# Performance work log

Measured on AMD Instinct MI355X. Metric: run time of the kernel, lower is better.

The kernel has to match this reference:

```python
import jax, jax.numpy as jnp
import numpy as np

N_TOKEN = 256
C_PAIR = 128
C = 32
N_HEADS = 4
LN_EPS = 1e-5


def setup_inputs() -> dict:
    key = jax.random.key(0)
    ks = jax.random.split(key, 8)
    w = lambda k, shape: jax.random.normal(k, shape, dtype=jnp.float32) * 0.02
    return {
        "pair": jax.random.normal(ks[0], (N_TOKEN, N_TOKEN, C_PAIR), dtype=jnp.float32),
        "gamma": jnp.ones((C_PAIR,), dtype=jnp.float32),
        "beta": jnp.zeros((C_PAIR,), dtype=jnp.float32),
        "Wq": w(ks[1], (C_PAIR, C * N_HEADS)),
        "Wk": w(ks[2], (C_PAIR, C * N_HEADS)),
        "Wv": w(ks[3], (C_PAIR, C * N_HEADS)),
        "Wb": w(ks[4], (C_PAIR, N_HEADS)),
        "Wg": w(ks[5], (C_PAIR, C * N_HEADS)),
        "Wout": w(ks[6], (C * N_HEADS, C_PAIR)),
    }


def _layernorm(x, gamma, beta):
    mu = jnp.mean(x, axis=-1, keepdims=True)
    var = jnp.mean(jnp.square(x - mu), axis=-1, keepdims=True)
    return (x - mu) * jax.lax.rsqrt(var + LN_EPS) * gamma + beta


def reference(pair, gamma, beta, Wq, Wk, Wv, Wb, Wg, Wout):
    n = pair.shape[0]
    pn = _layernorm(pair, gamma, beta)  # [N, N, c_pair]
    q = (pn @ Wq).reshape(n, n, N_HEADS, C)  # [i, j, h, c]
    k = (pn @ Wk).reshape(n, n, N_HEADS, C)  # [i, k, h, c]
    v = (pn @ Wv).reshape(n, n, N_HEADS, C)
    b = pn @ Wb                               # [j, k, h] pairwise bias
    g = jax.nn.sigmoid(pn @ Wg).reshape(n, n, N_HEADS, C)
    # a^h_ijk = softmax_k( q_ij . k_ik / sqrt(c) + b_jk )
    logits = jnp.einsum("ijhc,ikhc->ijkh", q, k) / np.float32(np.sqrt(C))
    logits = logits + b[None, :, :, :]        # broadcast over i: bias indexed by (j, k)
    attn = jax.nn.softmax(logits, axis=2)     # softmax over k axis
    o = jnp.einsum("ijkh,ikhc->ijhc", attn, v) * g
    return o.reshape(n, n, N_HEADS * C) @ Wout  # [N, N, c_pair]
```

## Files before the change

### kernel.cpp

```cpp
#include <hip/hip_runtime.h>

#define N_TOK 256
#define CP    128
#define CHD   32
#define NH    4
#define NT    65536
#define NCOL  528

typedef short short8 __attribute__((ext_vector_type(8)));
typedef float f32x4  __attribute__((ext_vector_type(4)));
typedef float f32x2  __attribute__((ext_vector_type(2)));

__device__ __forceinline__ short f2bf(float f) {
    unsigned u = __builtin_bit_cast(unsigned, f);
    u += 0x7fffu + ((u >> 16) & 1u);
    return (short)(u >> 16);
}
__device__ __forceinline__ float bf2f(short s) {
    unsigned u = ((unsigned)(unsigned short)s) << 16;
    return __builtin_bit_cast(float, u);
}

__global__ void pack_weights(const float* __restrict__ Wq, const float* __restrict__ Wk,
                             const float* __restrict__ Wv, const float* __restrict__ Wb,
                             const float* __restrict__ Wg, const float* __restrict__ Wout,
                             short* __restrict__ wcat, short* __restrict__ woutT) {
    int idx = blockIdx.x * 256 + threadIdx.x;
    if (idx < NCOL * CP) {
        int n = idx >> 7, k = idx & 127;
        float v = 0.f;
        if (n < 512) {
            const float* W = (n < 128) ? Wq : (n < 256) ? Wk : (n < 384) ? Wv : Wg;
            int col = (n & 96) + 2 * (n & 15) + ((n >> 4) & 1);
            v = W[k * 128 + col];
            if (n < 128) v *= 0.17677669529663687f;
        } else if (n < 516) {
            v = Wb[k * 4 + (n - 512)];
        }
        wcat[n * CP + k] = f2bf(v);
    } else {
        int j = idx - NCOL * CP;
        if (j < 128 * 128) {
            int n = j >> 7, k = j & 127;
            int col = (n & 96) + 2 * (n & 15) + ((n >> 4) & 1);
            woutT[n * 128 + k] = f2bf(Wout[k * 128 + col]);
        }
    }
}

__global__ __launch_bounds__(256, 4)
void ln_proj(const float* __restrict__ pair, const float* __restrict__ gamma,
             const float* __restrict__ beta, const short* __restrict__ wcat,
             short* __restrict__ qt, short* __restrict__ kt,
             short* __restrict__ vt, short* __restrict__ gt,
             float* __restrict__ bt) {
    __shared__ short pn[10240];
    const int tid = threadIdx.x;
    const int wv = tid >> 6, lane = tid & 63;
    const int quad = lane >> 4, l15 = lane & 15;
    const int r0 = blockIdx.x * 64;
    short* const ST = &pn[wv * 2560];

    float ga0 = gamma[2 * lane], ga1 = gamma[2 * lane + 1];
    float be0 = beta[2 * lane],  be1 = beta[2 * lane + 1];

    #pragma unroll 4
    for (int rr = 0; rr < 16; ++rr) {
        int row = wv * 16 + rr;
        const float* src = pair + (size_t)(r0 + row) * CP + 2 * lane;
        float x0 = src[0], x1 = src[1];
        float s = x0 + x1;
        #pragma unroll
        for (int m = 32; m; m >>= 1) s += __shfl_xor(s, m);
        float mu = s * (1.f / 128.f);
        float d0 = x0 - mu, d1 = x1 - mu;
        float vs = d0 * d0 + d1 * d1;
        #pragma unroll
        for (int m = 32; m; m >>= 1) vs += __shfl_xor(vs, m);
        float rs = rsqrtf(vs * (1.f / 128.f) + 1e-5f);
        short y0 = f2bf(d0 * rs * ga0 + be0);
        short y1 = f2bf(d1 * rs * ga1 + be1);
        unsigned pk = ((unsigned)(unsigned short)y0) | (((unsigned)(unsigned short)y1) << 16);
        *(unsigned*)&pn[row * 136 + 2 * lane] = pk;
    }
    __syncthreads();

    short8 af[4][4];
    #pragma unroll
    for (int rt = 0; rt < 4; ++rt)
        #pragma unroll
        for (int s = 0; s < 4; ++s)
            af[rt][s] = *(const short8*)&pn[(rt * 16 + l15) * 136 + s * 32 + quad * 8];
    __syncthreads();

    short* const dst = (wv == 0) ? qt : (wv == 1) ? kt : (wv == 2) ? vt : gt;

#define LOADB(BUF, CHN) {                                                          \
        int n_ = (CHN) * 16 + l15;                                                 \
        _Pragma("unroll")                                                          \
        for (int s = 0; s < 4; ++s)                                                \
            BUF[s] = *(const short8*)&wcat[(size_t)n_ * CP + s * 32 + quad * 8];   \
    }

#define EVEN(BUF) {                                                                \
        _Pragma("unroll")                                                          \
        for (int rt = 0; rt < 4; ++rt) {                                           \
            f32x4 a = {0.f, 0.f, 0.f, 0.f};                                        \
            _Pragma("unroll")                                                      \
            for (int s = 0; s < 4; ++s)                                            \
                a = __builtin_amdgcn_mfma_f32_16x16x32_bf16(af[rt][s], BUF[s], a, 0, 0, 0); \
            accE[rt] = a;                                                          \
        }                                                                          \
    }

#define ODD(CC, BUF) {                                                             \
        const int chn = wv * 8 + (CC);                                             \
        const int h_ = (chn >> 1) & 3;                                             \
        _Pragma("unroll")                                                          \
        for (int rt = 0; rt < 4; ++rt) {                                           \
            f32x4 a = {0.f, 0.f, 0.f, 0.f};                                        \
            _Pragma("unroll")                                                      \
            for (int s = 0; s < 4; ++s)                                            \
                a = __builtin_amdgcn_mfma_f32_16x16x32_bf16(af[rt][s], BUF[s], a, 0, 0, 0); \
            _Pragma("unroll")                                                      \
            for (int r = 0; r < 4; ++r) {                                          \
                int rowl = rt * 16 + quad * 4 + r;                                 \
                float ve = accE[rt][r], vo = a[r];                                 \
                if (wv == 3) {                                                     \
                    ve = 1.f / (1.f + __expf(-ve));                                \
                    vo = 1.f / (1.f + __expf(-vo));                                \
                }                                                                  \
                unsigned pk = ((unsigned)(unsigned short)f2bf(ve))                 \
                            | (((unsigned)(unsigned short)f2bf(vo)) << 16);        \
                *(unsigned*)&ST[rowl * 40 + 2 * l15] = pk;                         \
            }                                                                      \
        }                                                                          \
        const size_t hb2 = (size_t)h_ * NT * CHD + (size_t)r0 * CHD;               \
        _Pragma("unroll")                                                          \
        for (int s = 0; s < 4; ++s) {                                              \
            int f = s * 64 + lane;                                                 \
            int row = f >> 2, cs = (f & 3) * 8;                                    \
            short8 v = *(const short8*)&ST[row * 40 + cs];                         \
            *(short8*)(dst + hb2 + (size_t)row * CHD + cs) = v;                    \
        }                                                                          \
    }

    short8 bA[4], bB[4];
    f32x4 accE[4];
    LOADB(bA, wv * 8 + 0)
    LOADB(bB, wv * 8 + 1)
    EVEN(bA) LOADB(bA, wv * 8 + 2)
    ODD(1, bB) LOADB(bB, wv * 8 + 3)
    EVEN(bA) LOADB(bA, wv * 8 + 4)
    ODD(3, bB) LOADB(bB, wv * 8 + 5)
    EVEN(bA) LOADB(bA, wv * 8 + 6)
    ODD(5, bB) LOADB(bB, wv * 8 + 7)
    EVEN(bA) LOADB(bA, wv * 8 + 8)
    ODD(7, bB)

    if (wv == 3) {
        #pragma unroll
        for (int rt = 0; rt < 4; ++rt) {
            f32x4 acc = {0.f, 0.f, 0.f, 0.f};
            #pragma unroll
            for (int s = 0; s < 4; ++s)
                acc = __builtin_amdgcn_mfma_f32_16x16x32_bf16(af[rt][s], bA[s], acc, 0, 0, 0);
            if (l15 < 4) {
                #pragma unroll
                for (int r = 0; r < 4; ++r) {
                    int gr = r0 + rt * 16 + quad * 4 + r;
                    bt[l15 * NT + gr] = acc[r];
                }
            }
        }
    }
#undef LOADB
#undef EVEN
#undef ODD
}

__global__ __launch_bounds__(256)
void bias_T(const float* __restrict__ bt, float* __restrict__ btT) {
    __shared__ float t[64][65];
    int bid = blockIdx.x;
    int h = bid >> 4, tj = (bid >> 2) & 3, tk = bid & 3;
    const float* src = bt + (size_t)h * NT;
    float* dstp = btT + (size_t)h * NT;
    int c = threadIdx.x & 63, r4 = threadIdx.x >> 6;
    #pragma unroll
    for (int rr = 0; rr < 16; ++rr) {
        int r = rr * 4 + r4;
        t[r][c] = src[(size_t)(tj * 64 + r) * 256 + tk * 64 + c];
    }
    __syncthreads();
    #pragma unroll
    for (int rr = 0; rr < 16; ++rr) {
        int k = rr * 4 + r4;
        dstp[(size_t)(tk * 64 + k) * 256 + tj * 64 + c] = t[c][k];
    }
}

__global__ __launch_bounds__(256)
void attn(const short* __restrict__ qt, const short* __restrict__ kt,
          const short* __restrict__ vt, const short* __restrict__ gt,
          const float* __restrict__ btT, short* __restrict__ og) {
    __shared__ short vT[32 * 264];
    __shared__ short pl[64 * 264];
    const int tid = threadIdx.x;
    const int h = blockIdx.x >> 8, i = blockIdx.x & 255;
    const int wv = tid >> 6, lane = tid & 63;
    const int quad = lane >> 4, l15 = lane & 15;

    const short* kbase = kt + ((size_t)h * NT + (size_t)i * 256) * CHD;
    const short* vbase = vt + ((size_t)h * NT + (size_t)i * 256) * CHD;
    const short* qbase = qt + ((size_t)h * NT + (size_t)i * 256) * CHD;
    const short* gbase = gt + ((size_t)h * NT + (size_t)i * 256) * CHD;
    const float* btTb = btT + (size_t)h * NT;

    for (int g = tid; g < 1024; g += 256) {
        int key = g >> 2, p = g & 3;
        short8 s = *(const short8*)(vbase + key * CHD + p * 8);
        #pragma unroll
        for (int cc = 0; cc < 8; ++cc) {
            int c = p * 8 + cc;
            int row = (c & 1) ? 16 + (c >> 1) : (c >> 1);
            vT[row * 264 + key] = s[cc];
        }
    }
    __syncthreads();

    for (int jt = 0; jt < 4; ++jt) {
        int jbase = jt * 64 + wv * 16;
        short8 aq = *(const short8*)(qbase + (jbase + l15) * CHD + quad * 8);

        f32x4 sacc[16];
        __builtin_amdgcn_s_setprio(1);
        #pragma unroll
        for (int t = 0; t < 16; ++t) {
            f32x4 c = *(const f32x4*)(btTb + (size_t)(t * 16 + l15) * 256 + jbase + quad * 4);
            short8 bk = *(const short8*)(kbase + (t * 16 + l15) * CHD + quad * 8);
            sacc[t] = __builtin_amdgcn_mfma_f32_16x16x32_bf16(aq, bk, c, 0, 0, 0);
        }
        __builtin_amdgcn_s_setprio(0);
        float mx[4] = {-1e30f, -1e30f, -1e30f, -1e30f}, sm[4] = {0.f, 0.f, 0.f, 0.f};
        #pragma unroll
        for (int t = 0; t < 16; ++t)
            #pragma unroll
            for (int r = 0; r < 4; ++r) mx[r] = fmaxf(mx[r], sacc[t][r]);
        #pragma unroll
        for (int m = 1; m < 16; m <<= 1)
            #pragma unroll
            for (int r = 0; r < 4; ++r) mx[r] = fmaxf(mx[r], __shfl_xor(mx[r], m, 16));
        #pragma unroll
        for (int t = 0; t < 16; ++t)
            #pragma unroll
            for (int r = 0; r < 4; ++r) {
                float e = __expf(sacc[t][r] - mx[r]);
                sacc[t][r] = e;
                sm[r] += e;
            }
        #pragma unroll
        for (int m = 1; m < 16; m <<= 1)
            #pragma unroll
            for (int r = 0; r < 4; ++r) sm[r] += __shfl_xor(sm[r], m, 16);
        float inv[4];
        #pragma unroll
        for (int r = 0; r < 4; ++r) inv[r] = 1.f / sm[r];
        #pragma unroll
        for (int t = 0; t < 16; ++t)
            #pragma unroll
            for (int r = 0; r < 4; ++r)
                pl[(wv * 16 + quad * 4 + r) * 264 + t * 16 + l15] = f2bf(sacc[t][r] * inv[r]);
        f32x4 oacc[2];
        oacc[0] = f32x4{0.f, 0.f, 0.f, 0.f};
        oacc[1] = f32x4{0.f, 0.f, 0.f, 0.f};
        __builtin_amdgcn_s_setprio(1);
        #pragma unroll
        for (int ks = 0; ks < 8; ++ks) {
            short8 ap = *(const short8*)&pl[(wv * 16 + l15) * 264 + ks * 32 + quad * 8];
            #pragma unroll
            for (int nt = 0; nt < 2; ++nt) {
                short8 bv = *(const short8*)&vT[(nt * 16 + l15) * 264 + ks * 32 + quad * 8];
                oacc[nt] = __builtin_amdgcn_mfma_f32_16x16x32_bf16(ap, bv, oacc[nt], 0, 0, 0);
            }
        }
        __builtin_amdgcn_s_setprio(0);
        #pragma unroll
        for (int r = 0; r < 4; ++r) {
            int j = jbase + quad * 4 + r;
            unsigned gw = *(const unsigned*)(gbase + (size_t)j * CHD + 2 * l15);
            float g0 = bf2f((short)(gw & 0xffff));
            float g1 = bf2f((short)(gw >> 16));
            unsigned pk = ((unsigned)(unsigned short)f2bf(oacc[0][r] * g0))
                        | (((unsigned)(unsigned short)f2bf(oacc[1][r] * g1)) << 16);
            *(unsigned*)&og[((size_t)i * 256 + j) * CP + h * CHD + 2 * l15] = pk;
        }
    }
}

__global__ __launch_bounds__(256)
void out_gemm(const short* __restrict__ og, const short* __restrict__ woutT,
              float* __restrict__ out) {
    __shared__ short al[64 * 136];
    const int tid = threadIdx.x;
    const int wv = tid >> 6, lane = tid & 63;
    const int quad = lane >> 4, l15 = lane & 15;
    const int r0 = blockIdx.x * 64;

    for (int g = tid; g < 1024; g += 256) {
        int row = g >> 4, p = g & 15;
        *(short8*)&al[row * 136 + p * 8] = *(const short8*)(og + (size_t)(r0 + row) * CP + p * 8);
    }
    __syncthreads();

    short8 af[4][4];
    #pragma unroll
    for (int rt = 0; rt < 4; ++rt)
        #pragma unroll
        for (int s = 0; s < 4; ++s)
            af[rt][s] = *(const short8*)&al[(rt * 16 + l15) * 136 + s * 32 + quad * 8];

    short8 bE[4], bO[4];
    #pragma unroll
    for (int s = 0; s < 4; ++s) {
        bE[s] = *(const short8*)&woutT[(size_t)(wv * 32 + l15) * 128 + s * 32 + quad * 8];
        bO[s] = *(const short8*)&woutT[(size_t)(wv * 32 + 16 + l15) * 128 + s * 32 + quad * 8];
    }

    #pragma unroll
    for (int rt = 0; rt < 4; ++rt) {
        f32x4 accE = {0.f, 0.f, 0.f, 0.f}, accO = {0.f, 0.f, 0.f, 0.f};
        #pragma unroll
        for (int s = 0; s < 4; ++s) {
            accE = __builtin_amdgcn_mfma_f32_16x16x32_bf16(af[rt][s], bE[s], accE, 0, 0, 0);
            accO = __builtin_amdgcn_mfma_f32_16x16x32_bf16(af[rt][s], bO[s], accO, 0, 0, 0);
        }
        #pragma unroll
        for (int r = 0; r < 4; ++r) {
            f32x2 pk = {accE[r], accO[r]};
            *(f32x2*)&out[(size_t)(r0 + rt * 16 + quad * 4 + r) * CP + wv * 32 + 2 * l15] = pk;
        }
    }
}

extern "C" void kernel_launch(void* const* d_in, const int* in_sizes, int n_in,
                              void* d_out, int out_size, void* d_ws, size_t ws_size,
                              hipStream_t stream) {
    (void)in_sizes; (void)n_in; (void)out_size; (void)ws_size;
    const float* pair  = (const float*)d_in[0];
    const float* gamma = (const float*)d_in[1];
    const float* beta  = (const float*)d_in[2];
    const float* Wq    = (const float*)d_in[3];
    const float* Wk    = (const float*)d_in[4];
    const float* Wv    = (const float*)d_in[5];
    const float* Wb    = (const float*)d_in[6];
    const float* Wg    = (const float*)d_in[7];
    const float* Wout  = (const float*)d_in[8];
    float* out = (float*)d_out;

    char* ws = (char*)d_ws;
    const size_t SZ_QKVG = (size_t)NH * NT * CHD * 2;
    short* wcat  = (short*)(ws);
    short* woutT = (short*)(ws + 135168);
    short* qt    = (short*)(ws + 167936);
    short* kt    = (short*)(ws + 167936 + SZ_QKVG);
    short* vt    = (short*)(ws + 167936 + 2 * SZ_QKVG);
    short* gt    = (short*)(ws + 167936 + 3 * SZ_QKVG);
    float* bt    = (float*)(ws + 167936 + 4 * SZ_QKVG);
    float* btT   = (float*)(ws + 167936 + 4 * SZ_QKVG + (size_t)NH * NT * 4);
    short* og    = (short*)(ws + 167936 + 4 * SZ_QKVG + 2 * (size_t)NH * NT * 4);

    hipLaunchKernelGGL(pack_weights, dim3(328), dim3(256), 0, stream,
                       Wq, Wk, Wv, Wb, Wg, Wout, wcat, woutT);
    hipLaunchKernelGGL(ln_proj, dim3(1024), dim3(256), 0, stream,
                       pair, gamma, beta, wcat, qt, kt, vt, gt, bt);
    hipLaunchKernelGGL(bias_T, dim3(64), dim3(256), 0, stream, bt, btT);
    hipLaunchKernelGGL(attn, dim3(1024), dim3(256), 0, stream,
                       qt, kt, vt, gt, btT, og);
    hipLaunchKernelGGL(out_gemm, dim3(1024), dim3(256), 0, stream,
                       og, woutT, out);
}
```

Baseline: 195.9 us.

## Write V pre-transposed from projection kernel and drop LDS transpose in attention

The projection kernel now writes V in a transposed [h][i][c][k] layout, staged through a padded LDS tile (stride 42) to limit bank conflicts. The attention kernel then reads V B-fragments straight from global memory, so it no longer needs its vT LDS buffer, the per-block scatter transpose or the barrier. Less LDS also lets launch_bounds ask for 4 blocks per CU. The trade-off is uncoalesced 4-byte scattered stores in ln_proj and V reads that now come from global/L2 inside the PV loop rather than from LDS.

```diff
diff --git a/kernel.cpp b/kernel.cpp
--- a/kernel.cpp
+++ b/kernel.cpp
@@ -54,12 +54,13 @@
              short* __restrict__ qt, short* __restrict__ kt,
              short* __restrict__ vt, short* __restrict__ gt,
              float* __restrict__ bt) {
-    __shared__ short pn[10240];
+    __shared__ short pn[10752];
     const int tid = threadIdx.x;
     const int wv = tid >> 6, lane = tid & 63;
     const int quad = lane >> 4, l15 = lane & 15;
     const int r0 = blockIdx.x * 64;
-    short* const ST = &pn[wv * 2560];
+    short* const ST = &pn[wv * 2688];
+    const int sstr = (wv == 2) ? 42 : 40;
 
     float ga0 = gamma[2 * lane], ga1 = gamma[2 * lane + 1];
     float be0 = beta[2 * lane],  be1 = beta[2 * lane + 1];
@@ -132,16 +133,29 @@
                 }                                                                  \
                 unsigned pk = ((unsigned)(unsigned short)f2bf(ve))                 \
                             | (((unsigned)(unsigned short)f2bf(vo)) << 16);        \
-                *(unsigned*)&ST[rowl * 40 + 2 * l15] = pk;                         \
+                *(unsigned*)&ST[rowl * sstr + 2 * l15] = pk;                       \
             }                                                                      \
         }                                                                          \
-        const size_t hb2 = (size_t)h_ * NT * CHD + (size_t)r0 * CHD;               \
-        _Pragma("unroll")                                                          \
-        for (int s = 0; s < 4; ++s) {                                              \
-            int f = s * 64 + lane;                                                 \
-            int row = f >> 2, cs = (f & 3) * 8;                                    \
-            short8 v = *(const short8*)&ST[row * 40 + cs];                         \
-            *(short8*)(dst + hb2 + (size_t)row * CHD + cs) = v;                    \
+        if (wv == 2) {                                                             \
+            const size_t tb = (((size_t)h_ * 256 + (r0 >> 8)) * 32) * 256 + (r0 & 255); \
+            _Pragma("unroll")                                                      \
+            for (int s2 = 0; s2 < 16; ++s2) {                                      \
+                int p = s2 * 2 + (lane >> 5);                                      \
+                int cx = (p < 16) ? 2 * p : 2 * (p - 16) + 1;                      \
+                int kl = 2 * (lane & 31);                                          \
+                unsigned lo = (unsigned short)ST[kl * 42 + cx];                    \
+                unsigned hi = (unsigned short)ST[(kl + 1) * 42 + cx];              \
+                *(unsigned*)&dst[tb + (size_t)p * 256 + kl] = lo | (hi << 16);     \
+            }                                                                      \
+        } else {                                                                   \
+            const size_t hb2 = (size_t)h_ * NT * CHD + (size_t)r0 * CHD;           \
+            _Pragma("unroll")                                                      \
+            for (int s = 0; s < 4; ++s) {                                          \
+                int f = s * 64 + lane;                                             \
+                int row = f >> 2, cs = (f & 3) * 8;                                \
+                short8 v = *(const short8*)&ST[row * 40 + cs];                     \
+                *(short8*)(dst + hb2 + (size_t)row * CHD + cs) = v;                \
+            }                                                                      \
         }                                                                          \
     }
 
@@ -200,11 +214,10 @@
     }
 }
 
-__global__ __launch_bounds__(256)
+__global__ __launch_bounds__(256, 4)
 void attn(const short* __restrict__ qt, const short* __restrict__ kt,
           const short* __restrict__ vt, const short* __restrict__ gt,
           const float* __restrict__ btT, short* __restrict__ og) {
-    __shared__ short vT[32 * 264];
     __shared__ short pl[64 * 264];
     const int tid = threadIdx.x;
     const int h = blockIdx.x >> 8, i = blockIdx.x & 255;
@@ -212,22 +225,10 @@
     const int quad = lane >> 4, l15 = lane & 15;
 
     const short* kbase = kt + ((size_t)h * NT + (size_t)i * 256) * CHD;
-    const short* vbase = vt + ((size_t)h * NT + (size_t)i * 256) * CHD;
+    const short* vtb   = vt + (((size_t)h * 256 + i) * 32) * 256;
     const short* qbase = qt + ((size_t)h * NT + (size_t)i * 256) * CHD;
     const short* gbase = gt + ((size_t)h * NT + (size_t)i * 256) * CHD;
     const float* btTb = btT + (size_t)h * NT;
-
-    for (int g = tid; g < 1024; g += 256) {
-        int key = g >> 2, p = g & 3;
-        short8 s = *(const short8*)(vbase + key * CHD + p * 8);
-        #pragma unroll
-        for (int cc = 0; cc < 8; ++cc) {
-            int c = p * 8 + cc;
-            int row = (c & 1) ? 16 + (c >> 1) : (c >> 1);
-            vT[row * 264 + key] = s[cc];
-        }
-    }
-    __syncthreads();
 
     for (int jt = 0; jt < 4; ++jt) {
         int jbase = jt * 64 + wv * 16;
@@ -280,7 +281,7 @@
             short8 ap = *(const short8*)&pl[(wv * 16 + l15) * 264 + ks * 32 + quad * 8];
             #pragma unroll
             for (int nt = 0; nt < 2; ++nt) {
-                short8 bv = *(const short8*)&vT[(nt * 16 + l15) * 264 + ks * 32 + quad * 8];
+                short8 bv = *(const short8*)(vtb + (size_t)(nt * 16 + l15) * 256 + ks * 32 + quad * 8);
                 oacc[nt] = __builtin_amdgcn_mfma_f32_16x16x32_bf16(ap, bv, oacc[nt], 0, 0, 0);
             }
         }
```

Measured after the change: 251.0 us. 28.1% more time.
